# Kernel optimization log

Measured on AMD Instinct MI355X. Metric: run time of the kernel, lower is better.

## Reference

```python
import jax, jax.numpy as jnp
import numpy as np

B, S, HID = 1, 8192, 768
H, D = 12, 64          # num heads, head dim (HID = H*D)
W = 256                # one-sided attention window


def _shift_chunks(xc, C):
    # xc: [B, C, w, H, D] -> prev/next chunk copies padded with zeros
    prev = jnp.pad(xc, ((0, 0), (1, 0), (0, 0), (0, 0), (0, 0)))[:, :C]
    nxt = jnp.pad(xc, ((0, 0), (0, 1), (0, 0), (0, 0), (0, 0)))[:, 1:]
    return jnp.concatenate([prev, xc, nxt], axis=2)  # [B, C, 3w, H, D]


def sliding_window_attention(q, k, v, w):
    # q,k,v: [B, S, H, D]; q already scaled. Band width 2w+1.
    b, s, h, d = q.shape
    c = s // w
    qc = q.reshape(b, c, w, h, d)
    k3 = _shift_chunks(k.reshape(b, c, w, h, d), c)  # [b,c,3w,h,d]
    v3 = _shift_chunks(v.reshape(b, c, w, h, d), c)
    # scores of each query chunk against its 3-chunk key neighborhood
    scores3 = jnp.einsum('bcxhd,bcyhd->bhcxy', qc, k3)  # [b,h,c,w,3w]
    rows = jnp.arange(w)
    offs = jnp.arange(2 * w + 1)
    gidx = rows[:, None] + offs[None, :]  # [w, 2w+1] local key index p+j
    band = scores3[..., rows[:, None], gidx]  # [b,h,c,w,2w+1]
    # mask keys outside [0, S) (same effect as mask_invalid_locations)
    gq = jnp.arange(s).reshape(c, w)                    # global query pos
    keypos = gq[..., None] + (offs - w)                 # [c,w,2w+1]
    valid = (keypos >= 0) & (keypos < s)
    band = jnp.where(valid[None, None], band, -jnp.inf)
    prob = jax.nn.softmax(band, axis=-1)
    prob = jnp.where(valid[None, None], prob, 0.0)
    # scatter band probs back to 3w layout, then banded PV matmul
    prob3 = jnp.zeros(band.shape[:-1] + (3 * w,), band.dtype)
    prob3 = prob3.at[..., rows[:, None], gidx].set(prob)  # [b,h,c,w,3w]
    ctx = jnp.einsum('bhcxy,bcyhd->bcxhd', prob3, v3)
    return ctx.reshape(b, s, h, d)


def setup_inputs() -> dict:
    key = jax.random.key(0)
    ks = jax.random.split(key, 4)
    sc = 1.0 / np.sqrt(HID)
    return {
        'hidden_states': jax.random.normal(ks[0], (B, S, HID), jnp.float32),
        'Wq': jax.random.normal(ks[1], (HID, HID), jnp.float32) * sc,
        'bq': jnp.zeros((HID,), jnp.float32),
        'Wk': jax.random.normal(ks[2], (HID, HID), jnp.float32) * sc,
        'bk': jnp.zeros((HID,), jnp.float32),
        'Wv': jax.random.normal(ks[3], (HID, HID), jnp.float32) * sc,
        'bv': jnp.zeros((HID,), jnp.float32),
    }


def reference(hidden_states, Wq, bq, Wk, bk, Wv, bv):
    b, s, hid = hidden_states.shape
    q = (hidden_states @ Wq + bq).reshape(b, s, H, D)
    k = (hidden_states @ Wk + bk).reshape(b, s, H, D)
    v = (hidden_states @ Wv + bv).reshape(b, s, H, D)
    q = q / jnp.asarray(np.sqrt(D), q.dtype)
    ctx = sliding_window_attention(q, k, v, W)  # [b,s,H,D]
    return ctx.reshape(b, s, hid)
```

## Files before the change

### kernel.cpp

```cpp
#include <hip/hip_runtime.h>
#include <hip/hip_bf16.h>

#define S_LEN 8192
#define HID 768
#define NH 12
#define HD 64
#define WIN 256

typedef __bf16 bf16x8 __attribute__((ext_vector_type(8)));
typedef float f32x4 __attribute__((ext_vector_type(4)));
using bf16_t = __hip_bfloat16;

#define MFMA(a, b, c) __builtin_amdgcn_mfma_f32_16x16x32_bf16(a, b, c, 0, 0, 0)

__device__ __forceinline__ void gl2lds16(const bf16_t* g, bf16_t* l) {
  __builtin_amdgcn_global_load_lds(
      (const __attribute__((address_space(1))) void*)g,
      (__attribute__((address_space(3))) void*)l, 16, 0, 0);
}

__global__ __launch_bounds__(256) void conv_hs(const float* __restrict__ hs,
                                               bf16_t* __restrict__ hb) {
  int i = (blockIdx.x * 256 + threadIdx.x) * 4;
  float4 v = *reinterpret_cast<const float4*>(hs + i);
  union { ushort4 u; bf16_t b[4]; } H;
  H.b[0] = __float2bfloat16(v.x);
  H.b[1] = __float2bfloat16(v.y);
  H.b[2] = __float2bfloat16(v.z);
  H.b[3] = __float2bfloat16(v.w);
  *reinterpret_cast<ushort4*>(hb + i) = H.u;
}

__global__ __launch_bounds__(256) void transpose_w(const float* __restrict__ Wq,
                                                   const float* __restrict__ Wk,
                                                   const float* __restrict__ Wv,
                                                   bf16_t* __restrict__ Wt) {
  __shared__ float t[32][33];
  int z = blockIdx.z;
  const float* src = (z == 0) ? Wq : ((z == 1) ? Wk : Wv);
  int n0 = blockIdx.x * 32, k0 = blockIdx.y * 32;
  int tx = threadIdx.x, ty = threadIdx.y;
  for (int i = 0; i < 4; ++i)
    t[ty + i * 8][tx] = src[(k0 + ty + i * 8) * HID + n0 + tx];
  __syncthreads();
  bf16_t* dst = Wt + z * HID * HID;
  for (int i = 0; i < 4; ++i)
    dst[(n0 + ty + i * 8) * HID + k0 + tx] = __float2bfloat16(t[tx][ty + i * 8]);
}

__global__ __launch_bounds__(256) void qkv_gemm(
    const bf16_t* __restrict__ hb, const bf16_t* __restrict__ Wt,
    const float* __restrict__ bq, const float* __restrict__ bk,
    const float* __restrict__ bv,
    bf16_t* __restrict__ Qw, bf16_t* __restrict__ Kw, bf16_t* __restrict__ Vt) {
  __shared__ __align__(16) bf16_t sA[128 * 64];
  __shared__ __align__(16) bf16_t sB[128 * 64];
  int m0 = blockIdx.x * 128;
  int zq = blockIdx.y / 6;
  int nn0 = (blockIdx.y % 6) * 128;
  int n0g = zq * HID + nn0;
  int tid = threadIdx.x;
  int w = tid >> 6, lane = tid & 63, lm = lane & 15, qd = lane >> 4;
  int wm = w & 1, wn = w >> 1;

  int srow = w * 8 + (lane >> 3);
  int sc8 = (lane & 7) ^ ((lane >> 3) & 7);
  const bf16_t* gA = hb + (m0 + srow) * HID + sc8 * 8;
  const bf16_t* gB = Wt + (n0g + srow) * HID + sc8 * 8;
  int sx0 = lm & 7;

  f32x4 acc[4][4] = {};
  for (int kk = 0; kk < HID; kk += 64) {
#pragma unroll
    for (int u = 0; u < 4; ++u) {
      gl2lds16(gA + (u * 32) * HID + kk, sA + u * 2048 + w * 512);
      gl2lds16(gB + (u * 32) * HID + kk, sB + u * 2048 + w * 512);
    }
    __syncthreads();
#pragma unroll
    for (int half = 0; half < 2; ++half) {
      int ca = (qd + 4 * half) ^ sx0;
      bf16x8 fa[4], fb[4];
#pragma unroll
      for (int i = 0; i < 4; ++i) {
        fa[i] = *reinterpret_cast<const bf16x8*>(
            sA + (wm * 64 + i * 16 + lm) * 64 + ca * 8);
        fb[i] = *reinterpret_cast<const bf16x8*>(
            sB + (wn * 64 + i * 16 + lm) * 64 + ca * 8);
      }
      if (zq == 2) {
#pragma unroll
        for (int i = 0; i < 4; ++i)
#pragma unroll
          for (int j = 0; j < 4; ++j)
            acc[i][j] = MFMA(fb[i], fa[j], acc[i][j]);
      } else {
#pragma unroll
        for (int i = 0; i < 4; ++i)
#pragma unroll
          for (int j = 0; j < 4; ++j)
            acc[i][j] = MFMA(fa[i], fb[j], acc[i][j]);
      }
    }
    __syncthreads();
  }

  if (zq != 2) {
    const float* bias = zq ? bk : bq;
    bf16_t* dst = zq ? Kw : Qw;
    float scale = zq ? 1.0f : 0.125f;
#pragma unroll
    for (int j = 0; j < 4; ++j) {
      int nl = nn0 + wn * 64 + j * 16 + lm;
      float bb = bias[nl];
      int h = nl >> 6, d = nl & 63;
#pragma unroll
      for (int i = 0; i < 4; ++i)
#pragma unroll
        for (int r = 0; r < 4; ++r) {
          int m = m0 + wm * 64 + i * 16 + qd * 4 + r;
          dst[(h * S_LEN + m) * HD + d] =
              __float2bfloat16((acc[i][j][r] + bb) * scale);
        }
    }
  } else {
#pragma unroll
    for (int i = 0; i < 4; ++i)
#pragma unroll
      for (int r = 0; r < 4; ++r) {
        int nl = nn0 + wn * 64 + i * 16 + qd * 4 + r;
        float bb = bv[nl];
#pragma unroll
        for (int j = 0; j < 4; ++j) {
          int m = m0 + wm * 64 + j * 16 + lm;
          Vt[nl * S_LEN + m] = __float2bfloat16(acc[i][j][r] + bb);
        }
      }
  }
}

__global__ __launch_bounds__(256) void swa_kernel(
    const bf16_t* __restrict__ Qw, const bf16_t* __restrict__ Kw,
    const bf16_t* __restrict__ Vt, float* __restrict__ out) {
  __shared__ __align__(16) bf16_t sK[2][64 * 64];
  __shared__ __align__(16) bf16_t sV[2][64 * 64];
  __shared__ __align__(16) bf16_t sP[4 * 16 * 72];
  int h = blockIdx.y;
  int nb = blockIdx.x;
  int q0 = (((nb & 7) << 4) | (nb >> 3)) * 64;
  int tid = threadIdx.x;
  int w = tid >> 6, lane = tid & 63, lm = lane & 15, qd = lane >> 4;
  int xb = q0 + w * 16;

  int qoff = (h * S_LEN + xb + lm) * HD + qd * 8;
  bf16x8 aq0 = *reinterpret_cast<const bf16x8*>(Qw + qoff);
  bf16x8 aq1 = *reinterpret_cast<const bf16x8*>(Qw + qoff + 32);

  f32x4 o[4] = {};
  float lsum[4] = {0.f, 0.f, 0.f, 0.f};

  int y_begin = q0 - WIN; if (y_begin < 0) y_begin = 0;
  int y_end = q0 + 64 + WIN; if (y_end > S_LEN) y_end = S_LEN;
  int ntiles = (y_end - y_begin) >> 6;
  const bf16_t* Kh = Kw + h * S_LEN * HD;
  const bf16_t* Vh = Vt + h * HD * S_LEN;
  bf16_t* sPw = sP + w * 16 * 72;

  int srow = w * 8 + (lane >> 3);
  int sc8 = (lane & 7) ^ ((lane >> 3) & 7);
  int sx0 = lm & 7;

#define STAGE(y0, b)                                                    \
  {                                                                     \
    const bf16_t* kg = Kh + ((y0) + srow) * HD + sc8 * 8;               \
    gl2lds16(kg, &sK[b][w * 512]);                                      \
    gl2lds16(kg + 32 * HD, &sK[b][2048 + w * 512]);                     \
    const bf16_t* vg = Vh + srow * S_LEN + (y0) + sc8 * 8;              \
    gl2lds16(vg, &sV[b][w * 512]);                                      \
    gl2lds16(vg + 32 * S_LEN, &sV[b][2048 + w * 512]);                  \
  }

  STAGE(y_begin, 0);
  __syncthreads();

  for (int t = 0; t < ntiles; ++t) {
    int y0 = y_begin + t * 64;
    if (t + 1 < ntiles) STAGE(y0 + 64, (t + 1) & 1);
    int b = t & 1;
    f32x4 s[4] = {};
#pragma unroll
    for (int nt = 0; nt < 4; ++nt) {
      const bf16_t* kr = &sK[b][(nt * 16 + lm) * 64];
      bf16x8 b0 = *reinterpret_cast<const bf16x8*>(kr + (qd ^ sx0) * 8);
      bf16x8 b1 = *reinterpret_cast<const bf16x8*>(kr + ((qd + 4) ^ sx0) * 8);
      s[nt] = MFMA(aq0, b0, s[nt]);
      s[nt] = MFMA(aq1, b1, s[nt]);
    }
    int dy = y0 - q0;
    bool edge = (dy > 192) || (dy < -192);
#pragma unroll
    for (int nt = 0; nt < 4; ++nt) {
#pragma unroll
      for (int r = 0; r < 4; ++r) {
        float pv;
        if (edge) {
          int dlt = (y0 + nt * 16 + lm) - (xb + qd * 4 + r);
          pv = (dlt <= WIN && dlt >= -WIN) ? __expf(s[nt][r]) : 0.f;
        } else {
          pv = __expf(s[nt][r]);
        }
        bf16_t pb = __float2bfloat16(pv);
        lsum[r] += __bfloat162float(pb);
        sPw[(qd * 4 + r) * 72 + nt * 16 + lm] = pb;
      }
    }
    bf16x8 ap0 = *reinterpret_cast<const bf16x8*>(sPw + lm * 72 + qd * 8);
    bf16x8 ap1 = *reinterpret_cast<const bf16x8*>(sPw + lm * 72 + 32 + qd * 8);
#pragma unroll
    for (int nt = 0; nt < 4; ++nt) {
      const bf16_t* vr = &sV[b][(nt * 16 + lm) * 64];
      bf16x8 v0 = *reinterpret_cast<const bf16x8*>(vr + (qd ^ sx0) * 8);
      bf16x8 v1 = *reinterpret_cast<const bf16x8*>(vr + ((qd + 4) ^ sx0) * 8);
      o[nt] = MFMA(ap0, v0, o[nt]);
      o[nt] = MFMA(ap1, v1, o[nt]);
    }
    __syncthreads();
  }
#pragma unroll
  for (int r = 0; r < 4; ++r) {
    float v = lsum[r];
    v += __shfl_xor(v, 1);
    v += __shfl_xor(v, 2);
    v += __shfl_xor(v, 4);
    v += __shfl_xor(v, 8);
    float inv = 1.f / v;
    int x = xb + qd * 4 + r;
#pragma unroll
    for (int nt = 0; nt < 4; ++nt)
      out[x * HID + h * HD + nt * 16 + lm] = o[nt][r] * inv;
  }
}

extern "C" void kernel_launch(void* const* d_in, const int* in_sizes, int n_in,
                              void* d_out, int out_size, void* d_ws, size_t ws_size,
                              hipStream_t stream) {
  const float* hs = (const float*)d_in[0];
  const float* Wq = (const float*)d_in[1];
  const float* bq = (const float*)d_in[2];
  const float* Wk = (const float*)d_in[3];
  const float* bk = (const float*)d_in[4];
  const float* Wv = (const float*)d_in[5];
  const float* bv = (const float*)d_in[6];
  float* out = (float*)d_out;

  const int NSH = S_LEN * HID;
  const int NW = 3 * HID * HID;
  bf16_t* p = (bf16_t*)d_ws;
  bf16_t* hb = p; p += NSH;
  bf16_t* Wt = p; p += NW;
  bf16_t* Qw = p; p += NSH;
  bf16_t* Kw = p; p += NSH;
  bf16_t* Vt = p; p += NSH;

  conv_hs<<<dim3(NSH / 4 / 256), dim3(256), 0, stream>>>(hs, hb);
  transpose_w<<<dim3(24, 24, 3), dim3(32, 8), 0, stream>>>(Wq, Wk, Wv, Wt);
  qkv_gemm<<<dim3(64, 18), dim3(256), 0, stream>>>(
      hb, Wt, bq, bk, bv, Qw, Kw, Vt);
  swa_kernel<<<dim3(128, 12), dim3(256), 0, stream>>>(Qw, Kw, Vt, out);
}
```

Measured before the change: 175.1 us.

## Transpose MFMA operand order to vectorize projection stores and P writes

Swaps the MFMA A/B operands in the QKV projection and in the attention score computation, so each lane's four accumulator values run along a contiguous output dimension. The projection epilogue can then write packed 4-element bf16 stores with a float4 bias load, and the attention kernel writes P to LDS as a single 8-byte store per tile. The softmax row sum becomes one per-lane scalar reduced with two shuffles plus a broadcast. The sum now accumulates unrounded fp32 probabilities instead of bf16-rounded ones, which slightly changes numerics.

```diff
diff --git a/kernel.cpp b/kernel.cpp
--- a/kernel.cpp
+++ b/kernel.cpp
@@ -93,13 +93,13 @@
         for (int i = 0; i < 4; ++i)
 #pragma unroll
           for (int j = 0; j < 4; ++j)
+            acc[i][j] = MFMA(fa[i], fb[j], acc[i][j]);
+      } else {
+#pragma unroll
+        for (int i = 0; i < 4; ++i)
+#pragma unroll
+          for (int j = 0; j < 4; ++j)
             acc[i][j] = MFMA(fb[i], fa[j], acc[i][j]);
-      } else {
-#pragma unroll
-        for (int i = 0; i < 4; ++i)
-#pragma unroll
-          for (int j = 0; j < 4; ++j)
-            acc[i][j] = MFMA(fa[i], fb[j], acc[i][j]);
       }
     }
     __syncthreads();
@@ -110,32 +110,37 @@
     bf16_t* dst = zq ? Kw : Qw;
     float scale = zq ? 1.0f : 0.125f;
 #pragma unroll
-    for (int j = 0; j < 4; ++j) {
-      int nl = nn0 + wn * 64 + j * 16 + lm;
-      float bb = bias[nl];
-      int h = nl >> 6, d = nl & 63;
-#pragma unroll
-      for (int i = 0; i < 4; ++i)
-#pragma unroll
-        for (int r = 0; r < 4; ++r) {
-          int m = m0 + wm * 64 + i * 16 + qd * 4 + r;
-          dst[(h * S_LEN + m) * HD + d] =
-              __float2bfloat16((acc[i][j][r] + bb) * scale);
-        }
+    for (int i = 0; i < 4; ++i) {
+      int nbase = nn0 + wn * 64 + i * 16 + qd * 4;
+      float4 b4 = *reinterpret_cast<const float4*>(bias + nbase);
+      int h = nbase >> 6, d0 = nbase & 63;
+#pragma unroll
+      for (int j = 0; j < 4; ++j) {
+        int m = m0 + wm * 64 + j * 16 + lm;
+        union { ushort4 u; bf16_t b[4]; } P;
+        P.b[0] = __float2bfloat16((acc[i][j][0] + b4.x) * scale);
+        P.b[1] = __float2bfloat16((acc[i][j][1] + b4.y) * scale);
+        P.b[2] = __float2bfloat16((acc[i][j][2] + b4.z) * scale);
+        P.b[3] = __float2bfloat16((acc[i][j][3] + b4.w) * scale);
+        *reinterpret_cast<ushort4*>(dst + (h * S_LEN + m) * HD + d0) = P.u;
+      }
     }
   } else {
 #pragma unroll
-    for (int i = 0; i < 4; ++i)
-#pragma unroll
-      for (int r = 0; r < 4; ++r) {
-        int nl = nn0 + wn * 64 + i * 16 + qd * 4 + r;
+    for (int i = 0; i < 4; ++i) {
+      int mb = m0 + wm * 64 + i * 16 + qd * 4;
+#pragma unroll
+      for (int j = 0; j < 4; ++j) {
+        int nl = nn0 + wn * 64 + j * 16 + lm;
         float bb = bv[nl];
-#pragma unroll
-        for (int j = 0; j < 4; ++j) {
-          int m = m0 + wm * 64 + j * 16 + lm;
-          Vt[nl * S_LEN + m] = __float2bfloat16(acc[i][j][r] + bb);
-        }
-      }
+        union { ushort4 u; bf16_t b[4]; } P;
+        P.b[0] = __float2bfloat16(acc[i][j][0] + bb);
+        P.b[1] = __float2bfloat16(acc[i][j][1] + bb);
+        P.b[2] = __float2bfloat16(acc[i][j][2] + bb);
+        P.b[3] = __float2bfloat16(acc[i][j][3] + bb);
+        *reinterpret_cast<ushort4*>(Vt + nl * S_LEN + mb) = P.u;
+      }
+    }
   }
 }
 
@@ -157,7 +162,7 @@
   bf16x8 aq1 = *reinterpret_cast<const bf16x8*>(Qw + qoff + 32);
 
   f32x4 o[4] = {};
-  float lsum[4] = {0.f, 0.f, 0.f, 0.f};
+  float lsum = 0.f;
 
   int y_begin = q0 - WIN; if (y_begin < 0) y_begin = 0;
   int y_end = q0 + 64 + WIN; if (y_end > S_LEN) y_end = S_LEN;
@@ -193,26 +198,27 @@
       const bf16_t* kr = &sK[b][(nt * 16 + lm) * 64];
       bf16x8 b0 = *reinterpret_cast<const bf16x8*>(kr + (qd ^ sx0) * 8);
       bf16x8 b1 = *reinterpret_cast<const bf16x8*>(kr + ((qd + 4) ^ sx0) * 8);
-      s[nt] = MFMA(aq0, b0, s[nt]);
-      s[nt] = MFMA(aq1, b1, s[nt]);
+      s[nt] = MFMA(b0, aq0, s[nt]);
+      s[nt] = MFMA(b1, aq1, s[nt]);
     }
     int dy = y0 - q0;
     bool edge = (dy > 192) || (dy < -192);
 #pragma unroll
     for (int nt = 0; nt < 4; ++nt) {
+      union { ushort4 u; bf16_t b[4]; } P;
 #pragma unroll
       for (int r = 0; r < 4; ++r) {
         float pv;
         if (edge) {
-          int dlt = (y0 + nt * 16 + lm) - (xb + qd * 4 + r);
+          int dlt = (y0 + nt * 16 + qd * 4 + r) - (xb + lm);
           pv = (dlt <= WIN && dlt >= -WIN) ? __expf(s[nt][r]) : 0.f;
         } else {
           pv = __expf(s[nt][r]);
         }
-        bf16_t pb = __float2bfloat16(pv);
-        lsum[r] += __bfloat162float(pb);
-        sPw[(qd * 4 + r) * 72 + nt * 16 + lm] = pb;
-      }
+        lsum += pv;
+        P.b[r] = __float2bfloat16(pv);
+      }
+      *reinterpret_cast<ushort4*>(sPw + lm * 72 + nt * 16 + qd * 4) = P.u;
     }
     bf16x8 ap0 = *reinterpret_cast<const bf16x8*>(sPw + lm * 72 + qd * 8);
     bf16x8 ap1 = *reinterpret_cast<const bf16x8*>(sPw + lm * 72 + 32 + qd * 8);
@@ -226,14 +232,11 @@
     }
     __syncthreads();
   }
+  lsum += __shfl_xor(lsum, 16);
+  lsum += __shfl_xor(lsum, 32);
 #pragma unroll
   for (int r = 0; r < 4; ++r) {
-    float v = lsum[r];
-    v += __shfl_xor(v, 1);
-    v += __shfl_xor(v, 2);
-    v += __shfl_xor(v, 4);
-    v += __shfl_xor(v, 8);
-    float inv = 1.f / v;
+    float inv = 1.f / __shfl(lsum, qd * 4 + r);
     int x = xb + qd * 4 + r;
 #pragma unroll
     for (int nt = 0; nt < 4; ++nt)
```

Result: no change. 177.3 us (+1.2%).

## Load K/V fragments directly into registers, drop LDS staging and barriers

Applied to the files above, without the earlier changes.

The sliding-window attention kernel no longer stages K and V tiles through shared memory with async global-to-LDS copies and block barriers. Each wave now loads its K and V MFMA fragments straight from global memory into registers, with K double-buffered one tile ahead. The QK product is computed transposed so each lane holds one query's scores, which lets the row sum be a single per-lane accumulator and lets P be written to LDS as 8-byte vector stores with a padded stride. The trade-off is that the four waves no longer share K/V data, so each wave does redundant global or L2 traffic, and register pressure rises under the new occupancy hint.

```diff
diff --git a/kernel.cpp b/kernel.cpp
--- a/kernel.cpp
+++ b/kernel.cpp
@@ -139,12 +139,11 @@
   }
 }
 
-__global__ __launch_bounds__(256) void swa_kernel(
+#define PST 76
+__global__ __launch_bounds__(256, 2) void swa_kernel(
     const bf16_t* __restrict__ Qw, const bf16_t* __restrict__ Kw,
     const bf16_t* __restrict__ Vt, float* __restrict__ out) {
-  __shared__ __align__(16) bf16_t sK[2][64 * 64];
-  __shared__ __align__(16) bf16_t sV[2][64 * 64];
-  __shared__ __align__(16) bf16_t sP[4 * 16 * 72];
+  __shared__ __align__(16) bf16_t sP[4 * 16 * PST];
   int h = blockIdx.y;
   int nb = blockIdx.x;
   int q0 = (((nb & 7) << 4) | (nb >> 3)) * 64;
@@ -157,83 +156,77 @@
   bf16x8 aq1 = *reinterpret_cast<const bf16x8*>(Qw + qoff + 32);
 
   f32x4 o[4] = {};
-  float lsum[4] = {0.f, 0.f, 0.f, 0.f};
+  float lsum = 0.f;
 
   int y_begin = q0 - WIN; if (y_begin < 0) y_begin = 0;
   int y_end = q0 + 64 + WIN; if (y_end > S_LEN) y_end = S_LEN;
   int ntiles = (y_end - y_begin) >> 6;
   const bf16_t* Kh = Kw + h * S_LEN * HD;
   const bf16_t* Vh = Vt + h * HD * S_LEN;
-  bf16_t* sPw = sP + w * 16 * 72;
-
-  int srow = w * 8 + (lane >> 3);
-  int sc8 = (lane & 7) ^ ((lane >> 3) & 7);
-  int sx0 = lm & 7;
-
-#define STAGE(y0, b)                                                    \
-  {                                                                     \
-    const bf16_t* kg = Kh + ((y0) + srow) * HD + sc8 * 8;               \
-    gl2lds16(kg, &sK[b][w * 512]);                                      \
-    gl2lds16(kg + 32 * HD, &sK[b][2048 + w * 512]);                     \
-    const bf16_t* vg = Vh + srow * S_LEN + (y0) + sc8 * 8;              \
-    gl2lds16(vg, &sV[b][w * 512]);                                      \
-    gl2lds16(vg + 32 * S_LEN, &sV[b][2048 + w * 512]);                  \
-  }
-
-  STAGE(y_begin, 0);
-  __syncthreads();
-
+  bf16_t* sPw = sP + w * 16 * PST;
+
+  bf16x8 kf[2][4][2];
+#define LOADK(buf, y0)                                                   \
+  {                                                                      \
+    _Pragma("unroll") for (int nt = 0; nt < 4; ++nt) {                   \
+      const bf16_t* kr = Kh + ((y0) + nt * 16 + lm) * HD + qd * 8;       \
+      kf[buf][nt][0] = *reinterpret_cast<const bf16x8*>(kr);             \
+      kf[buf][nt][1] = *reinterpret_cast<const bf16x8*>(kr + 32);        \
+    }                                                                    \
+  }
+
+  LOADK(0, y_begin);
+
+#pragma unroll 2
   for (int t = 0; t < ntiles; ++t) {
     int y0 = y_begin + t * 64;
-    if (t + 1 < ntiles) STAGE(y0 + 64, (t + 1) & 1);
-    int b = t & 1;
+    int cur = t & 1;
+    if (t + 1 < ntiles) LOADK(cur ^ 1, y0 + 64);
+    bf16x8 vf[4][2];
+#pragma unroll
+    for (int nt = 0; nt < 4; ++nt) {
+      const bf16_t* vr = Vh + (nt * 16 + lm) * S_LEN + y0 + qd * 8;
+      vf[nt][0] = *reinterpret_cast<const bf16x8*>(vr);
+      vf[nt][1] = *reinterpret_cast<const bf16x8*>(vr + 32);
+    }
     f32x4 s[4] = {};
 #pragma unroll
     for (int nt = 0; nt < 4; ++nt) {
-      const bf16_t* kr = &sK[b][(nt * 16 + lm) * 64];
-      bf16x8 b0 = *reinterpret_cast<const bf16x8*>(kr + (qd ^ sx0) * 8);
-      bf16x8 b1 = *reinterpret_cast<const bf16x8*>(kr + ((qd + 4) ^ sx0) * 8);
-      s[nt] = MFMA(aq0, b0, s[nt]);
-      s[nt] = MFMA(aq1, b1, s[nt]);
+      s[nt] = MFMA(kf[cur][nt][0], aq0, s[nt]);
+      s[nt] = MFMA(kf[cur][nt][1], aq1, s[nt]);
     }
     int dy = y0 - q0;
     bool edge = (dy > 192) || (dy < -192);
 #pragma unroll
     for (int nt = 0; nt < 4; ++nt) {
+      union { ushort4 u; bf16_t b[4]; } P;
 #pragma unroll
       for (int r = 0; r < 4; ++r) {
         float pv;
         if (edge) {
-          int dlt = (y0 + nt * 16 + lm) - (xb + qd * 4 + r);
+          int dlt = (y0 + nt * 16 + qd * 4 + r) - (xb + lm);
           pv = (dlt <= WIN && dlt >= -WIN) ? __expf(s[nt][r]) : 0.f;
         } else {
           pv = __expf(s[nt][r]);
         }
-        bf16_t pb = __float2bfloat16(pv);
-        lsum[r] += __bfloat162float(pb);
-        sPw[(qd * 4 + r) * 72 + nt * 16 + lm] = pb;
-      }
-    }
-    bf16x8 ap0 = *reinterpret_cast<const bf16x8*>(sPw + lm * 72 + qd * 8);
-    bf16x8 ap1 = *reinterpret_cast<const bf16x8*>(sPw + lm * 72 + 32 + qd * 8);
-#pragma unroll
-    for (int nt = 0; nt < 4; ++nt) {
-      const bf16_t* vr = &sV[b][(nt * 16 + lm) * 64];
-      bf16x8 v0 = *reinterpret_cast<const bf16x8*>(vr + (qd ^ sx0) * 8);
-      bf16x8 v1 = *reinterpret_cast<const bf16x8*>(vr + ((qd + 4) ^ sx0) * 8);
-      o[nt] = MFMA(ap0, v0, o[nt]);
-      o[nt] = MFMA(ap1, v1, o[nt]);
-    }
-    __syncthreads();
-  }
+        lsum += pv;
+        P.b[r] = __float2bfloat16(pv);
+      }
+      *reinterpret_cast<ushort4*>(sPw + lm * PST + nt * 16 + qd * 4) = P.u;
+    }
+    bf16x8 ap0 = *reinterpret_cast<const bf16x8*>(sPw + lm * PST + qd * 8);
+    bf16x8 ap1 = *reinterpret_cast<const bf16x8*>(sPw + lm * PST + 32 + qd * 8);
+#pragma unroll
+    for (int nt = 0; nt < 4; ++nt) {
+      o[nt] = MFMA(ap0, vf[nt][0], o[nt]);
+      o[nt] = MFMA(ap1, vf[nt][1], o[nt]);
+    }
+  }
+  lsum += __shfl_xor(lsum, 16);
+  lsum += __shfl_xor(lsum, 32);
 #pragma unroll
   for (int r = 0; r < 4; ++r) {
-    float v = lsum[r];
-    v += __shfl_xor(v, 1);
-    v += __shfl_xor(v, 2);
-    v += __shfl_xor(v, 4);
-    v += __shfl_xor(v, 8);
-    float inv = 1.f / v;
+    float inv = 1.f / __shfl(lsum, qd * 4 + r);
     int x = xb + qd * 4 + r;
 #pragma unroll
     for (int nt = 0; nt < 4; ++nt)
```

Result: slower. 305.8 us (+74.6%).
